# Kernel optimization log

Measured on AMD Instinct MI355X. Metric: run time of the kernel, lower is better.

## Reference

```python
import jax, jax.numpy as jnp
import numpy as np


def _procrustes_align(X, Y):
    """Batched similarity-transform (scipy-style Procrustes, reflection allowed).
    Aligns Y (pred) to X (target). X, Y: [B, N, 3]. Returns aligned Y: [B, N, 3].
    """
    muX = X.mean(axis=1, keepdims=True)                      # [B,1,3]
    muY = Y.mean(axis=1, keepdims=True)
    X0 = X - muX
    Y0 = Y - muY
    normX = jnp.sqrt((X0 ** 2).sum(axis=(1, 2), keepdims=True))  # [B,1,1]
    normY = jnp.sqrt((Y0 ** 2).sum(axis=(1, 2), keepdims=True))
    X0n = X0 / normX
    Y0n = Y0 / normY
    # 3x3 cross-covariance per batch element
    M = jnp.einsum('bni,bnj->bij', X0n, Y0n)                 # [B,3,3]
    U, s, Vt = jnp.linalg.svd(M)                             # batched tiny SVD
    # Optimal rotation Q = V @ U^T = (U @ Vt)^T  (minimizes ||Y0n @ Q - X0n||)
    Q = jnp.swapaxes(jnp.matmul(U, Vt), -1, -2)              # [B,3,3]
    traceTA = s.sum(-1)[:, None, None]                       # [B,1,1]
    Z = normX * traceTA * jnp.einsum('bni,bij->bnj', Y0n, Q) + muX
    return Z


def setup_inputs() -> dict:
    key = jax.random.key(0)
    k1, k2 = jax.random.split(key)
    B, N = 262144, 21
    pred_kp3d = jax.random.normal(k1, (B, N, 3), dtype=jnp.float32)
    target_kp3d = jax.random.normal(k2, (B, N, 3), dtype=jnp.float32)
    return {"pred_kp3d": pred_kp3d, "target_kp3d": target_kp3d}


def reference(pred_kp3d, target_kp3d):
    pred_aligned = _procrustes_align(target_kp3d, pred_kp3d)
    # mean per-joint Euclidean distance (PA-MPJPE style)
    err = jnp.sqrt(((pred_aligned - target_kp3d) ** 2).sum(-1)).mean()
    return err
```

## Files before the change

### kernel.cpp

```cpp
#include <hip/hip_runtime.h>
#include <math.h>

#define NPTS 21
#define FLB  63
#define BPB  64
#define THREADS 64
#define NVEC (BPB * FLB / 4)
#define FULL_ROUNDS (NVEC / THREADS)
#define TAIL_LANES  (NVEC % THREADS)

__device__ __forceinline__ void async_cp16(const float* g, float* l) {
    __builtin_amdgcn_global_load_lds(
        (__attribute__((address_space(1))) void*)g,
        (__attribute__((address_space(3))) void*)l,
        16, 0, 0);
}

__global__ __launch_bounds__(THREADS, 3)
void pa_mpjpe(const float* __restrict__ pred,
              const float* __restrict__ targ,
              float* __restrict__ ws,
              int B)
{
    __shared__ __align__(16) float sbuf[BPB * FLB];

    const int tid = threadIdx.x;
    const int b0  = blockIdx.x * BPB;

    {
        const float* gp = pred + (size_t)b0 * FLB;
        #pragma unroll
        for (int j = 0; j < FULL_ROUNDS; ++j)
            async_cp16(gp + 4 * (j * THREADS + tid), sbuf + 4 * (j * THREADS));
        if (tid < TAIL_LANES)
            async_cp16(gp + 4 * (FULL_ROUNDS * THREADS + tid),
                       sbuf + 4 * (FULL_ROUNDS * THREADS));
    }
    __builtin_amdgcn_s_waitcnt(0x0F70);
    __syncthreads();

    float y[NPTS][3];
    float sy0 = 0.f, sy1 = 0.f, sy2 = 0.f, syy = 0.f;
    const int base = tid * FLB;
    #pragma unroll
    for (int n = 0; n < NPTS; ++n) {
        float a = sbuf[base + 3*n + 0];
        float b = sbuf[base + 3*n + 1];
        float c = sbuf[base + 3*n + 2];
        y[n][0] = a; y[n][1] = b; y[n][2] = c;
        sy0 += a; sy1 += b; sy2 += c;
        syy = fmaf(a, a, fmaf(b, b, fmaf(c, c, syy)));
    }
    __syncthreads();

    {
        const float* gt = targ + (size_t)b0 * FLB;
        #pragma unroll
        for (int j = 0; j < FULL_ROUNDS; ++j)
            async_cp16(gt + 4 * (j * THREADS + tid), sbuf + 4 * (j * THREADS));
        if (tid < TAIL_LANES)
            async_cp16(gt + 4 * (FULL_ROUNDS * THREADS + tid),
                       sbuf + 4 * (FULL_ROUNDS * THREADS));
    }
    __builtin_amdgcn_s_waitcnt(0x0F70);
    __syncthreads();

    float sx0 = 0.f, sx1 = 0.f, sx2 = 0.f;
    float m00=0,m01=0,m02=0, m10=0,m11=0,m12=0, m20=0,m21=0,m22=0;
    #pragma unroll
    for (int n = 0; n < NPTS; ++n) {
        float a = sbuf[base + 3*n + 0];
        float b = sbuf[base + 3*n + 1];
        float c = sbuf[base + 3*n + 2];
        sx0 += a; sx1 += b; sx2 += c;
        float u = y[n][0], v = y[n][1], w = y[n][2];
        m00 = fmaf(a,u,m00); m01 = fmaf(a,v,m01); m02 = fmaf(a,w,m02);
        m10 = fmaf(b,u,m10); m11 = fmaf(b,v,m11); m12 = fmaf(b,w,m12);
        m20 = fmaf(c,u,m20); m21 = fmaf(c,v,m21); m22 = fmaf(c,w,m22);
    }

    const float invN = 1.0f / (float)NPTS;
    float mux0 = sx0*invN, mux1 = sx1*invN, mux2 = sx2*invN;
    float muy0 = sy0*invN, muy1 = sy1*invN, muy2 = sy2*invN;
    float ny2  = syy - (sy0*sy0 + sy1*sy1 + sy2*sy2) * invN;
    float c00 = m00 - sx0*sy0*invN, c01 = m01 - sx0*sy1*invN, c02 = m02 - sx0*sy2*invN;
    float c10 = m10 - sx1*sy0*invN, c11 = m11 - sx1*sy1*invN, c12 = m12 - sx1*sy2*invN;
    float c20 = m20 - sx2*sy0*invN, c21 = m21 - sx2*sy1*invN, c22 = m22 - sx2*sy2*invN;

    float q00=c00, q01=c10, q02=c20,
          q10=c01, q11=c11, q12=c21,
          q20=c02, q21=c12, q22=c22;
    #pragma unroll
    for (int it = 0; it < 8; ++it) {
        float C00 = q11*q22 - q12*q21;
        float C01 = q12*q20 - q10*q22;
        float C02 = q10*q21 - q11*q20;
        float C10 = q02*q21 - q01*q22;
        float C11 = q00*q22 - q02*q20;
        float C12 = q01*q20 - q00*q21;
        float C20 = q01*q12 - q02*q11;
        float C21 = q02*q10 - q00*q12;
        float C22 = q00*q11 - q01*q10;
        float det = q00*C00 + q01*C01 + q02*C02;
        float ad  = fmaxf(fabsf(det), 1e-30f);
        float sdet = copysignf(ad, det);
        float g  = __expf(0.333333333f * __logf(ad));
        float ha = 0.5f / g;
        float hb = 0.5f * g / sdet;
        q00 = ha*q00 + hb*C00; q01 = ha*q01 + hb*C01; q02 = ha*q02 + hb*C02;
        q10 = ha*q10 + hb*C10; q11 = ha*q11 + hb*C11; q12 = ha*q12 + hb*C12;
        q20 = ha*q20 + hb*C20; q21 = ha*q21 + hb*C21; q22 = ha*q22 + hb*C22;
    }

    float trP = q00*c00 + q01*c10 + q02*c20
              + q10*c01 + q11*c11 + q12*c21
              + q20*c02 + q21*c12 + q22*c22;
    float k = trP / ny2;
    float r00=k*q00, r01=k*q01, r02=k*q02;
    float r10=k*q10, r11=k*q11, r12=k*q12;
    float r20=k*q20, r21=k*q21, r22=k*q22;

    float errsum = 0.0f;
    #pragma unroll
    for (int n = 0; n < NPTS; ++n) {
        float xa = sbuf[base + 3*n + 0];
        float xb = sbuf[base + 3*n + 1];
        float xc = sbuf[base + 3*n + 2];
        float u = y[n][0] - muy0, v = y[n][1] - muy1, w = y[n][2] - muy2;
        float z0 = fmaf(u, r00, fmaf(v, r10, fmaf(w, r20, mux0))) - xa;
        float z1 = fmaf(u, r01, fmaf(v, r11, fmaf(w, r21, mux1))) - xb;
        float z2 = fmaf(u, r02, fmaf(v, r12, fmaf(w, r22, mux2))) - xc;
        errsum += sqrtf(fmaf(z0, z0, fmaf(z1, z1, z2*z2)));
    }

    #pragma unroll
    for (int off = 32; off > 0; off >>= 1) errsum += __shfl_down(errsum, off, 64);
    if (tid == 0) ws[blockIdx.x] = errsum;
}

__global__ __launch_bounds__(256)
void pa_reduce(const float* __restrict__ ws, float* __restrict__ out,
               int nblk, float inv_total)
{
    __shared__ float sw[4];
    float s = 0.0f;
    for (int i = threadIdx.x; i < nblk; i += 256) s += ws[i];
    #pragma unroll
    for (int off = 32; off > 0; off >>= 1) s += __shfl_down(s, off, 64);
    if ((threadIdx.x & 63) == 0) sw[threadIdx.x >> 6] = s;
    __syncthreads();
    if (threadIdx.x == 0)
        out[0] = (sw[0] + sw[1] + sw[2] + sw[3]) * inv_total;
}

extern "C" void kernel_launch(void* const* d_in, const int* in_sizes, int n_in,
                              void* d_out, int out_size, void* d_ws, size_t ws_size,
                              hipStream_t stream)
{
    const float* pred = (const float*)d_in[0];
    const float* targ = (const float*)d_in[1];
    float* out = (float*)d_out;
    float* ws  = (float*)d_ws;

    int B = in_sizes[0] / FLB;
    int grid = (B + BPB - 1) / BPB;
    float inv_total = 1.0f / ((float)B * (float)NPTS);

    pa_mpjpe<<<grid, THREADS, 0, stream>>>(pred, targ, ws, B);
    pa_reduce<<<1, 256, 0, stream>>>(ws, out, grid, inv_total);
}
```

Measured before the change: 151.0 us.

## Use persistent grid with double-buffered async LDS prefetch of next chunk

Turns the kernel into a persistent grid of fixed size where each block loops over chunks. Pred and target each get their own LDS buffer, and the next chunk's loads are issued async while the current chunk is being computed, with explicit vmcnt waits. The aim is to hide global load latency behind compute and to cut block launch overhead. In exchange LDS per block doubles, occupancy drops (launch bounds 3 to 2), and correctness now depends on hand-tuned waitcnt values.

```diff
diff --git a/kernel.cpp b/kernel.cpp
--- a/kernel.cpp
+++ b/kernel.cpp
@@ -8,134 +8,147 @@
 #define NVEC (BPB * FLB / 4)
 #define FULL_ROUNDS (NVEC / THREADS)
 #define TAIL_LANES  (NVEC % THREADS)
+#define GRID 1280
 
-__device__ __forceinline__ void async_cp16(const float* g, float* l) {
-    __builtin_amdgcn_global_load_lds(
-        (__attribute__((address_space(1))) void*)g,
-        (__attribute__((address_space(3))) void*)l,
-        16, 0, 0);
+typedef __attribute__((address_space(3))) float       lds_f;
+typedef __attribute__((address_space(3))) void        lds_v;
+typedef const __attribute__((address_space(1))) void  gbl_v;
+
+__device__ __forceinline__ void async_cp16(const float* g, lds_f* l) {
+    __builtin_amdgcn_global_load_lds((gbl_v*)g, (lds_v*)l, 16, 0, 0);
 }
 
-__global__ __launch_bounds__(THREADS, 3)
+__device__ __forceinline__ void stage_chunk(const float* gbase, lds_f* lbuf, int tid) {
+    #pragma unroll
+    for (int j = 0; j < FULL_ROUNDS; ++j)
+        async_cp16(gbase + 4 * (j * THREADS + tid), lbuf + 4 * (j * THREADS));
+    if (tid < TAIL_LANES)
+        async_cp16(gbase + 4 * (FULL_ROUNDS * THREADS + tid),
+                   lbuf + 4 * (FULL_ROUNDS * THREADS));
+}
+
+__global__ __launch_bounds__(THREADS, 2)
 void pa_mpjpe(const float* __restrict__ pred,
               const float* __restrict__ targ,
               float* __restrict__ ws,
-              int B)
+              int nchunk)
 {
-    __shared__ __align__(16) float sbuf[BPB * FLB];
+    __shared__ __align__(16) float sp_[BPB * FLB];
+    __shared__ __align__(16) float st_[BPB * FLB];
+    lds_f* sp = (lds_f*)sp_;
+    lds_f* st = (lds_f*)st_;
 
-    const int tid = threadIdx.x;
-    const int b0  = blockIdx.x * BPB;
+    const int tid  = threadIdx.x;
+    const int base = tid * FLB;
+    const float invN = 1.0f / (float)NPTS;
+    float block_err = 0.0f;
 
-    {
-        const float* gp = pred + (size_t)b0 * FLB;
-        #pragma unroll
-        for (int j = 0; j < FULL_ROUNDS; ++j)
-            async_cp16(gp + 4 * (j * THREADS + tid), sbuf + 4 * (j * THREADS));
-        if (tid < TAIL_LANES)
-            async_cp16(gp + 4 * (FULL_ROUNDS * THREADS + tid),
-                       sbuf + 4 * (FULL_ROUNDS * THREADS));
-    }
-    __builtin_amdgcn_s_waitcnt(0x0F70);
-    __syncthreads();
-
-    float y[NPTS][3];
-    float sy0 = 0.f, sy1 = 0.f, sy2 = 0.f, syy = 0.f;
-    const int base = tid * FLB;
-    #pragma unroll
-    for (int n = 0; n < NPTS; ++n) {
-        float a = sbuf[base + 3*n + 0];
-        float b = sbuf[base + 3*n + 1];
-        float c = sbuf[base + 3*n + 2];
-        y[n][0] = a; y[n][1] = b; y[n][2] = c;
-        sy0 += a; sy1 += b; sy2 += c;
-        syy = fmaf(a, a, fmaf(b, b, fmaf(c, c, syy)));
-    }
-    __syncthreads();
-
-    {
-        const float* gt = targ + (size_t)b0 * FLB;
-        #pragma unroll
-        for (int j = 0; j < FULL_ROUNDS; ++j)
-            async_cp16(gt + 4 * (j * THREADS + tid), sbuf + 4 * (j * THREADS));
-        if (tid < TAIL_LANES)
-            async_cp16(gt + 4 * (FULL_ROUNDS * THREADS + tid),
-                       sbuf + 4 * (FULL_ROUNDS * THREADS));
-    }
-    __builtin_amdgcn_s_waitcnt(0x0F70);
-    __syncthreads();
-
-    float sx0 = 0.f, sx1 = 0.f, sx2 = 0.f;
-    float m00=0,m01=0,m02=0, m10=0,m11=0,m12=0, m20=0,m21=0,m22=0;
-    #pragma unroll
-    for (int n = 0; n < NPTS; ++n) {
-        float a = sbuf[base + 3*n + 0];
-        float b = sbuf[base + 3*n + 1];
-        float c = sbuf[base + 3*n + 2];
-        sx0 += a; sx1 += b; sx2 += c;
-        float u = y[n][0], v = y[n][1], w = y[n][2];
-        m00 = fmaf(a,u,m00); m01 = fmaf(a,v,m01); m02 = fmaf(a,w,m02);
-        m10 = fmaf(b,u,m10); m11 = fmaf(b,v,m11); m12 = fmaf(b,w,m12);
-        m20 = fmaf(c,u,m20); m21 = fmaf(c,v,m21); m22 = fmaf(c,w,m22);
+    int c = blockIdx.x;
+    if (c < nchunk) {
+        stage_chunk(pred + (size_t)c * (BPB * FLB), sp, tid);
+        stage_chunk(targ + (size_t)c * (BPB * FLB), st, tid);
     }
 
-    const float invN = 1.0f / (float)NPTS;
-    float mux0 = sx0*invN, mux1 = sx1*invN, mux2 = sx2*invN;
-    float muy0 = sy0*invN, muy1 = sy1*invN, muy2 = sy2*invN;
-    float ny2  = syy - (sy0*sy0 + sy1*sy1 + sy2*sy2) * invN;
-    float c00 = m00 - sx0*sy0*invN, c01 = m01 - sx0*sy1*invN, c02 = m02 - sx0*sy2*invN;
-    float c10 = m10 - sx1*sy0*invN, c11 = m11 - sx1*sy1*invN, c12 = m12 - sx1*sy2*invN;
-    float c20 = m20 - sx2*sy0*invN, c21 = m21 - sx2*sy1*invN, c22 = m22 - sx2*sy2*invN;
+    for (; c < nchunk; c += GRID) {
+        const int cn = c + GRID;
 
-    float q00=c00, q01=c10, q02=c20,
-          q10=c01, q11=c11, q12=c21,
-          q20=c02, q21=c12, q22=c22;
-    #pragma unroll
-    for (int it = 0; it < 8; ++it) {
-        float C00 = q11*q22 - q12*q21;
-        float C01 = q12*q20 - q10*q22;
-        float C02 = q10*q21 - q11*q20;
-        float C10 = q02*q21 - q01*q22;
-        float C11 = q00*q22 - q02*q20;
-        float C12 = q01*q20 - q00*q21;
-        float C20 = q01*q12 - q02*q11;
-        float C21 = q02*q10 - q00*q12;
-        float C22 = q00*q11 - q01*q10;
-        float det = q00*C00 + q01*C01 + q02*C02;
-        float ad  = fmaxf(fabsf(det), 1e-30f);
-        float sdet = copysignf(ad, det);
-        float g  = __expf(0.333333333f * __logf(ad));
-        float ha = 0.5f / g;
-        float hb = 0.5f * g / sdet;
-        q00 = ha*q00 + hb*C00; q01 = ha*q01 + hb*C01; q02 = ha*q02 + hb*C02;
-        q10 = ha*q10 + hb*C10; q11 = ha*q11 + hb*C11; q12 = ha*q12 + hb*C12;
-        q20 = ha*q20 + hb*C20; q21 = ha*q21 + hb*C21; q22 = ha*q22 + hb*C22;
-    }
+        asm volatile("s_waitcnt vmcnt(16)" ::: "memory");
 
-    float trP = q00*c00 + q01*c10 + q02*c20
-              + q10*c01 + q11*c11 + q12*c21
-              + q20*c02 + q21*c12 + q22*c22;
-    float k = trP / ny2;
-    float r00=k*q00, r01=k*q01, r02=k*q02;
-    float r10=k*q10, r11=k*q11, r12=k*q12;
-    float r20=k*q20, r21=k*q21, r22=k*q22;
+        float y[NPTS][3];
+        float sy0 = 0.f, sy1 = 0.f, sy2 = 0.f, syy = 0.f;
+        #pragma unroll
+        for (int n = 0; n < NPTS; ++n) {
+            float a = sp[base + 3*n + 0];
+            float b = sp[base + 3*n + 1];
+            float d = sp[base + 3*n + 2];
+            y[n][0] = a; y[n][1] = b; y[n][2] = d;
+            sy0 += a; sy1 += b; sy2 += d;
+            syy = fmaf(a, a, fmaf(b, b, fmaf(d, d, syy)));
+        }
+        asm volatile("s_waitcnt lgkmcnt(0)" ::: "memory");
+        if (cn < nchunk) {
+            stage_chunk(pred + (size_t)cn * (BPB * FLB), sp, tid);
+            asm volatile("s_waitcnt vmcnt(16)" ::: "memory");
+        } else {
+            asm volatile("s_waitcnt vmcnt(0)" ::: "memory");
+        }
 
-    float errsum = 0.0f;
-    #pragma unroll
-    for (int n = 0; n < NPTS; ++n) {
-        float xa = sbuf[base + 3*n + 0];
-        float xb = sbuf[base + 3*n + 1];
-        float xc = sbuf[base + 3*n + 2];
-        float u = y[n][0] - muy0, v = y[n][1] - muy1, w = y[n][2] - muy2;
-        float z0 = fmaf(u, r00, fmaf(v, r10, fmaf(w, r20, mux0))) - xa;
-        float z1 = fmaf(u, r01, fmaf(v, r11, fmaf(w, r21, mux1))) - xb;
-        float z2 = fmaf(u, r02, fmaf(v, r12, fmaf(w, r22, mux2))) - xc;
-        errsum += sqrtf(fmaf(z0, z0, fmaf(z1, z1, z2*z2)));
+        float sx0 = 0.f, sx1 = 0.f, sx2 = 0.f;
+        float m00=0,m01=0,m02=0, m10=0,m11=0,m12=0, m20=0,m21=0,m22=0;
+        #pragma unroll
+        for (int n = 0; n < NPTS; ++n) {
+            float a = st[base + 3*n + 0];
+            float b = st[base + 3*n + 1];
+            float d = st[base + 3*n + 2];
+            sx0 += a; sx1 += b; sx2 += d;
+            float u = y[n][0], v = y[n][1], w = y[n][2];
+            m00 = fmaf(a,u,m00); m01 = fmaf(a,v,m01); m02 = fmaf(a,w,m02);
+            m10 = fmaf(b,u,m10); m11 = fmaf(b,v,m11); m12 = fmaf(b,w,m12);
+            m20 = fmaf(d,u,m20); m21 = fmaf(d,v,m21); m22 = fmaf(d,w,m22);
+        }
+
+        float mux0 = sx0*invN, mux1 = sx1*invN, mux2 = sx2*invN;
+        float muy0 = sy0*invN, muy1 = sy1*invN, muy2 = sy2*invN;
+        float ny2  = syy - (sy0*sy0 + sy1*sy1 + sy2*sy2) * invN;
+        float c00 = m00 - sx0*sy0*invN, c01 = m01 - sx0*sy1*invN, c02 = m02 - sx0*sy2*invN;
+        float c10 = m10 - sx1*sy0*invN, c11 = m11 - sx1*sy1*invN, c12 = m12 - sx1*sy2*invN;
+        float c20 = m20 - sx2*sy0*invN, c21 = m21 - sx2*sy1*invN, c22 = m22 - sx2*sy2*invN;
+
+        float q00=c00, q01=c10, q02=c20,
+              q10=c01, q11=c11, q12=c21,
+              q20=c02, q21=c12, q22=c22;
+        #pragma unroll
+        for (int it = 0; it < 8; ++it) {
+            float C00 = q11*q22 - q12*q21;
+            float C01 = q12*q20 - q10*q22;
+            float C02 = q10*q21 - q11*q20;
+            float C10 = q02*q21 - q01*q22;
+            float C11 = q00*q22 - q02*q20;
+            float C12 = q01*q20 - q00*q21;
+            float C20 = q01*q12 - q02*q11;
+            float C21 = q02*q10 - q00*q12;
+            float C22 = q00*q11 - q01*q10;
+            float det = q00*C00 + q01*C01 + q02*C02;
+            float ad  = fmaxf(fabsf(det), 1e-30f);
+            float sdet = copysignf(ad, det);
+            float g  = __expf(0.333333333f * __logf(ad));
+            float ha = 0.5f / g;
+            float hb = 0.5f * g / sdet;
+            q00 = ha*q00 + hb*C00; q01 = ha*q01 + hb*C01; q02 = ha*q02 + hb*C02;
+            q10 = ha*q10 + hb*C10; q11 = ha*q11 + hb*C11; q12 = ha*q12 + hb*C12;
+            q20 = ha*q20 + hb*C20; q21 = ha*q21 + hb*C21; q22 = ha*q22 + hb*C22;
+        }
+
+        float trP = q00*c00 + q01*c10 + q02*c20
+                  + q10*c01 + q11*c11 + q12*c21
+                  + q20*c02 + q21*c12 + q22*c22;
+        float k = trP / ny2;
+        float r00=k*q00, r01=k*q01, r02=k*q02;
+        float r10=k*q10, r11=k*q11, r12=k*q12;
+        float r20=k*q20, r21=k*q21, r22=k*q22;
+
+        float errsum = 0.0f;
+        #pragma unroll
+        for (int n = 0; n < NPTS; ++n) {
+            float xa = st[base + 3*n + 0];
+            float xb = st[base + 3*n + 1];
+            float xc = st[base + 3*n + 2];
+            float u = y[n][0] - muy0, v = y[n][1] - muy1, w = y[n][2] - muy2;
+            float z0 = fmaf(u, r00, fmaf(v, r10, fmaf(w, r20, mux0))) - xa;
+            float z1 = fmaf(u, r01, fmaf(v, r11, fmaf(w, r21, mux1))) - xb;
+            float z2 = fmaf(u, r02, fmaf(v, r12, fmaf(w, r22, mux2))) - xc;
+            errsum += sqrtf(fmaf(z0, z0, fmaf(z1, z1, z2*z2)));
+        }
+        block_err += errsum;
+
+        asm volatile("s_waitcnt lgkmcnt(0)" ::: "memory");
+        if (cn < nchunk)
+            stage_chunk(targ + (size_t)cn * (BPB * FLB), st, tid);
     }
 
     #pragma unroll
-    for (int off = 32; off > 0; off >>= 1) errsum += __shfl_down(errsum, off, 64);
-    if (tid == 0) ws[blockIdx.x] = errsum;
+    for (int off = 32; off > 0; off >>= 1) block_err += __shfl_down(block_err, off, 64);
+    if (tid == 0) ws[blockIdx.x] = block_err;
 }
 
 __global__ __launch_bounds__(256)
@@ -163,9 +176,9 @@
     float* ws  = (float*)d_ws;
 
     int B = in_sizes[0] / FLB;
-    int grid = (B + BPB - 1) / BPB;
+    int nchunk = B / BPB;
     float inv_total = 1.0f / ((float)B * (float)NPTS);
 
-    pa_mpjpe<<<grid, THREADS, 0, stream>>>(pred, targ, ws, B);
-    pa_reduce<<<1, 256, 0, stream>>>(ws, out, grid, inv_total);
+    pa_mpjpe<<<GRID, THREADS, 0, stream>>>(pred, targ, ws, nchunk);
+    pa_reduce<<<1, 256, 0, stream>>>(ws, out, GRID, inv_total);
 }
```

Result: slower. 160.0 us (+6.0%).

## Load each batch element directly into registers instead of staging through LDS

Applied to the files above, without the earlier changes.

Drops the shared-memory staging with async global-to-LDS copies. Each thread now reads its own 63-float pred and target records straight into registers with 16-byte vector loads, and the block barriers go away. Per-lane loads are strided by 252 bytes, so coalescing gets worse, and holding 126 floats per thread raises register pressure. The launch-bounds occupancy hint drops from 3 to 2.

```diff
diff --git a/kernel.cpp b/kernel.cpp
--- a/kernel.cpp
+++ b/kernel.cpp
@@ -3,139 +3,104 @@
 
 #define NPTS 21
 #define FLB  63
-#define BPB  64
-#define THREADS 64
-#define NVEC (BPB * FLB / 4)
-#define FULL_ROUNDS (NVEC / THREADS)
-#define TAIL_LANES  (NVEC % THREADS)
 
-__device__ __forceinline__ void async_cp16(const float* g, float* l) {
-    __builtin_amdgcn_global_load_lds(
-        (__attribute__((address_space(1))) void*)g,
-        (__attribute__((address_space(3))) void*)l,
-        16, 0, 0);
-}
-
-__global__ __launch_bounds__(THREADS, 3)
+__global__ __launch_bounds__(64, 2)
 void pa_mpjpe(const float* __restrict__ pred,
               const float* __restrict__ targ,
               float* __restrict__ ws,
               int B)
 {
-    __shared__ __align__(16) float sbuf[BPB * FLB];
+    const int b = blockIdx.x * 64 + threadIdx.x;
+    float errsum = 0.0f;
 
-    const int tid = threadIdx.x;
-    const int b0  = blockIdx.x * BPB;
+    if (b < B) {
+        const float* gp = pred + (size_t)b * FLB;
+        const float* gt = targ + (size_t)b * FLB;
 
-    {
-        const float* gp = pred + (size_t)b0 * FLB;
+        float yv[FLB];
+        float xv[FLB];
         #pragma unroll
-        for (int j = 0; j < FULL_ROUNDS; ++j)
-            async_cp16(gp + 4 * (j * THREADS + tid), sbuf + 4 * (j * THREADS));
-        if (tid < TAIL_LANES)
-            async_cp16(gp + 4 * (FULL_ROUNDS * THREADS + tid),
-                       sbuf + 4 * (FULL_ROUNDS * THREADS));
-    }
-    __builtin_amdgcn_s_waitcnt(0x0F70);
-    __syncthreads();
+        for (int i = 0; i < 15; ++i) __builtin_memcpy(&yv[4*i], gp + 4*i, 16);
+        __builtin_memcpy(&yv[60], gp + 60, 12);
+        #pragma unroll
+        for (int i = 0; i < 15; ++i) __builtin_memcpy(&xv[4*i], gt + 4*i, 16);
+        __builtin_memcpy(&xv[60], gt + 60, 12);
 
-    float y[NPTS][3];
-    float sy0 = 0.f, sy1 = 0.f, sy2 = 0.f, syy = 0.f;
-    const int base = tid * FLB;
-    #pragma unroll
-    for (int n = 0; n < NPTS; ++n) {
-        float a = sbuf[base + 3*n + 0];
-        float b = sbuf[base + 3*n + 1];
-        float c = sbuf[base + 3*n + 2];
-        y[n][0] = a; y[n][1] = b; y[n][2] = c;
-        sy0 += a; sy1 += b; sy2 += c;
-        syy = fmaf(a, a, fmaf(b, b, fmaf(c, c, syy)));
-    }
-    __syncthreads();
+        float sy0 = 0.f, sy1 = 0.f, sy2 = 0.f, syy = 0.f;
+        #pragma unroll
+        for (int n = 0; n < NPTS; ++n) {
+            float a = yv[3*n+0], bb = yv[3*n+1], d = yv[3*n+2];
+            sy0 += a; sy1 += bb; sy2 += d;
+            syy = fmaf(a, a, fmaf(bb, bb, fmaf(d, d, syy)));
+        }
 
-    {
-        const float* gt = targ + (size_t)b0 * FLB;
+        float sx0 = 0.f, sx1 = 0.f, sx2 = 0.f;
+        float m00=0,m01=0,m02=0, m10=0,m11=0,m12=0, m20=0,m21=0,m22=0;
         #pragma unroll
-        for (int j = 0; j < FULL_ROUNDS; ++j)
-            async_cp16(gt + 4 * (j * THREADS + tid), sbuf + 4 * (j * THREADS));
-        if (tid < TAIL_LANES)
-            async_cp16(gt + 4 * (FULL_ROUNDS * THREADS + tid),
-                       sbuf + 4 * (FULL_ROUNDS * THREADS));
-    }
-    __builtin_amdgcn_s_waitcnt(0x0F70);
-    __syncthreads();
+        for (int n = 0; n < NPTS; ++n) {
+            float a = xv[3*n+0], bb = xv[3*n+1], d = xv[3*n+2];
+            float u = yv[3*n+0], v = yv[3*n+1], w = yv[3*n+2];
+            sx0 += a; sx1 += bb; sx2 += d;
+            m00 = fmaf(a,u,m00); m01 = fmaf(a,v,m01); m02 = fmaf(a,w,m02);
+            m10 = fmaf(bb,u,m10); m11 = fmaf(bb,v,m11); m12 = fmaf(bb,w,m12);
+            m20 = fmaf(d,u,m20); m21 = fmaf(d,v,m21); m22 = fmaf(d,w,m22);
+        }
 
-    float sx0 = 0.f, sx1 = 0.f, sx2 = 0.f;
-    float m00=0,m01=0,m02=0, m10=0,m11=0,m12=0, m20=0,m21=0,m22=0;
-    #pragma unroll
-    for (int n = 0; n < NPTS; ++n) {
-        float a = sbuf[base + 3*n + 0];
-        float b = sbuf[base + 3*n + 1];
-        float c = sbuf[base + 3*n + 2];
-        sx0 += a; sx1 += b; sx2 += c;
-        float u = y[n][0], v = y[n][1], w = y[n][2];
-        m00 = fmaf(a,u,m00); m01 = fmaf(a,v,m01); m02 = fmaf(a,w,m02);
-        m10 = fmaf(b,u,m10); m11 = fmaf(b,v,m11); m12 = fmaf(b,w,m12);
-        m20 = fmaf(c,u,m20); m21 = fmaf(c,v,m21); m22 = fmaf(c,w,m22);
-    }
+        const float invN = 1.0f / (float)NPTS;
+        float mux0 = sx0*invN, mux1 = sx1*invN, mux2 = sx2*invN;
+        float muy0 = sy0*invN, muy1 = sy1*invN, muy2 = sy2*invN;
+        float ny2  = syy - (sy0*sy0 + sy1*sy1 + sy2*sy2) * invN;
+        float c00 = m00 - sx0*sy0*invN, c01 = m01 - sx0*sy1*invN, c02 = m02 - sx0*sy2*invN;
+        float c10 = m10 - sx1*sy0*invN, c11 = m11 - sx1*sy1*invN, c12 = m12 - sx1*sy2*invN;
+        float c20 = m20 - sx2*sy0*invN, c21 = m21 - sx2*sy1*invN, c22 = m22 - sx2*sy2*invN;
 
-    const float invN = 1.0f / (float)NPTS;
-    float mux0 = sx0*invN, mux1 = sx1*invN, mux2 = sx2*invN;
-    float muy0 = sy0*invN, muy1 = sy1*invN, muy2 = sy2*invN;
-    float ny2  = syy - (sy0*sy0 + sy1*sy1 + sy2*sy2) * invN;
-    float c00 = m00 - sx0*sy0*invN, c01 = m01 - sx0*sy1*invN, c02 = m02 - sx0*sy2*invN;
-    float c10 = m10 - sx1*sy0*invN, c11 = m11 - sx1*sy1*invN, c12 = m12 - sx1*sy2*invN;
-    float c20 = m20 - sx2*sy0*invN, c21 = m21 - sx2*sy1*invN, c22 = m22 - sx2*sy2*invN;
+        float q00=c00, q01=c10, q02=c20,
+              q10=c01, q11=c11, q12=c21,
+              q20=c02, q21=c12, q22=c22;
+        #pragma unroll
+        for (int it = 0; it < 8; ++it) {
+            float C00 = q11*q22 - q12*q21;
+            float C01 = q12*q20 - q10*q22;
+            float C02 = q10*q21 - q11*q20;
+            float C10 = q02*q21 - q01*q22;
+            float C11 = q00*q22 - q02*q20;
+            float C12 = q01*q20 - q00*q21;
+            float C20 = q01*q12 - q02*q11;
+            float C21 = q02*q10 - q00*q12;
+            float C22 = q00*q11 - q01*q10;
+            float det = q00*C00 + q01*C01 + q02*C02;
+            float ad  = fmaxf(fabsf(det), 1e-30f);
+            float sdet = copysignf(ad, det);
+            float g  = __expf(0.333333333f * __logf(ad));
+            float ha = 0.5f / g;
+            float hb = 0.5f * g / sdet;
+            q00 = ha*q00 + hb*C00; q01 = ha*q01 + hb*C01; q02 = ha*q02 + hb*C02;
+            q10 = ha*q10 + hb*C10; q11 = ha*q11 + hb*C11; q12 = ha*q12 + hb*C12;
+            q20 = ha*q20 + hb*C20; q21 = ha*q21 + hb*C21; q22 = ha*q22 + hb*C22;
+        }
 
-    float q00=c00, q01=c10, q02=c20,
-          q10=c01, q11=c11, q12=c21,
-          q20=c02, q21=c12, q22=c22;
-    #pragma unroll
-    for (int it = 0; it < 8; ++it) {
-        float C00 = q11*q22 - q12*q21;
-        float C01 = q12*q20 - q10*q22;
-        float C02 = q10*q21 - q11*q20;
-        float C10 = q02*q21 - q01*q22;
-        float C11 = q00*q22 - q02*q20;
-        float C12 = q01*q20 - q00*q21;
-        float C20 = q01*q12 - q02*q11;
-        float C21 = q02*q10 - q00*q12;
-        float C22 = q00*q11 - q01*q10;
-        float det = q00*C00 + q01*C01 + q02*C02;
-        float ad  = fmaxf(fabsf(det), 1e-30f);
-        float sdet = copysignf(ad, det);
-        float g  = __expf(0.333333333f * __logf(ad));
-        float ha = 0.5f / g;
-        float hb = 0.5f * g / sdet;
-        q00 = ha*q00 + hb*C00; q01 = ha*q01 + hb*C01; q02 = ha*q02 + hb*C02;
-        q10 = ha*q10 + hb*C10; q11 = ha*q11 + hb*C11; q12 = ha*q12 + hb*C12;
-        q20 = ha*q20 + hb*C20; q21 = ha*q21 + hb*C21; q22 = ha*q22 + hb*C22;
-    }
+        float trP = q00*c00 + q01*c10 + q02*c20
+                  + q10*c01 + q11*c11 + q12*c21
+                  + q20*c02 + q21*c12 + q22*c22;
+        float k = trP / ny2;
+        float r00=k*q00, r01=k*q01, r02=k*q02;
+        float r10=k*q10, r11=k*q11, r12=k*q12;
+        float r20=k*q20, r21=k*q21, r22=k*q22;
 
-    float trP = q00*c00 + q01*c10 + q02*c20
-              + q10*c01 + q11*c11 + q12*c21
-              + q20*c02 + q21*c12 + q22*c22;
-    float k = trP / ny2;
-    float r00=k*q00, r01=k*q01, r02=k*q02;
-    float r10=k*q10, r11=k*q11, r12=k*q12;
-    float r20=k*q20, r21=k*q21, r22=k*q22;
-
-    float errsum = 0.0f;
-    #pragma unroll
-    for (int n = 0; n < NPTS; ++n) {
-        float xa = sbuf[base + 3*n + 0];
-        float xb = sbuf[base + 3*n + 1];
-        float xc = sbuf[base + 3*n + 2];
-        float u = y[n][0] - muy0, v = y[n][1] - muy1, w = y[n][2] - muy2;
-        float z0 = fmaf(u, r00, fmaf(v, r10, fmaf(w, r20, mux0))) - xa;
-        float z1 = fmaf(u, r01, fmaf(v, r11, fmaf(w, r21, mux1))) - xb;
-        float z2 = fmaf(u, r02, fmaf(v, r12, fmaf(w, r22, mux2))) - xc;
-        errsum += sqrtf(fmaf(z0, z0, fmaf(z1, z1, z2*z2)));
+        #pragma unroll
+        for (int n = 0; n < NPTS; ++n) {
+            float xa = xv[3*n+0], xb = xv[3*n+1], xc = xv[3*n+2];
+            float u = yv[3*n+0] - muy0, v = yv[3*n+1] - muy1, w = yv[3*n+2] - muy2;
+            float z0 = fmaf(u, r00, fmaf(v, r10, fmaf(w, r20, mux0))) - xa;
+            float z1 = fmaf(u, r01, fmaf(v, r11, fmaf(w, r21, mux1))) - xb;
+            float z2 = fmaf(u, r02, fmaf(v, r12, fmaf(w, r22, mux2))) - xc;
+            errsum += sqrtf(fmaf(z0, z0, fmaf(z1, z1, z2*z2)));
+        }
     }
 
     #pragma unroll
     for (int off = 32; off > 0; off >>= 1) errsum += __shfl_down(errsum, off, 64);
-    if (tid == 0) ws[blockIdx.x] = errsum;
+    if (threadIdx.x == 0) ws[blockIdx.x] = errsum;
 }
 
 __global__ __launch_bounds__(256)
@@ -163,9 +128,9 @@
     float* ws  = (float*)d_ws;
 
     int B = in_sizes[0] / FLB;
-    int grid = (B + BPB - 1) / BPB;
+    int grid = (B + 63) / 64;
     float inv_total = 1.0f / ((float)B * (float)NPTS);
 
-    pa_mpjpe<<<grid, THREADS, 0, stream>>>(pred, targ, ws, B);
+    pa_mpjpe<<<grid, 64, 0, stream>>>(pred, targ, ws, B);
     pa_reduce<<<1, 256, 0, stream>>>(ws, out, grid, inv_total);
 }
```

Measured after the change: 159.9 us. 1.06x slower.
